# Kernel optimization log

Measured on AMD Instinct MI355X. Metric: run time of the kernel, lower is better.

Reference implementation:

```python
import jax, jax.numpy as jnp
import numpy as np

D_MODEL = 1024
NUM_HEADS = 16
NUM_KV_HEADS = 4
HEAD_DIM = D_MODEL // NUM_HEADS  # 64
THETA = 10000.0
MAX_SEQ_LEN = 4096


def _rope_tables(max_seq_len, d_k, theta):
    k_vec = jnp.arange(0, d_k, 2, dtype=jnp.float32) / d_k
    freq = 1.0 / (theta ** k_vec)                       # (d_k/2,)
    ang = jnp.arange(max_seq_len, dtype=jnp.float32)[:, None] * freq[None, :]
    return jnp.cos(ang), jnp.sin(ang)                   # each (max_seq_len, d_k/2)


def _apply_rope(x, pos, cos_table, sin_table):
    # x: (b, h, l, d), pos: (b, l)
    cos = cos_table[pos][:, None, :, :]                 # (b, 1, l, d/2)
    sin = sin_table[pos][:, None, :, :]
    even, odd = x[..., 0::2], x[..., 1::2]
    r1 = even * cos - odd * sin
    r2 = even * sin + odd * cos
    return jnp.stack([r1, r2], axis=-1).reshape(x.shape)  # interleave back


def setup_inputs() -> dict:
    key = jax.random.key(0)
    ks = jax.random.split(key, 6)
    B, L, D = 1, 4096, D_MODEL
    std = (2.0 / (D + D)) ** 0.5
    std_kv = (2.0 / (D + HEAD_DIM * NUM_KV_HEADS)) ** 0.5
    x = jax.random.normal(ks[0], (B, L, D), dtype=jnp.float32)
    Wq = jax.random.normal(ks[1], (D, D), dtype=jnp.float32) * std
    Wk = jax.random.normal(ks[2], (HEAD_DIM * NUM_KV_HEADS, D), dtype=jnp.float32) * std_kv
    Wv = jax.random.normal(ks[3], (HEAD_DIM * NUM_KV_HEADS, D), dtype=jnp.float32) * std_kv
    Wo = jax.random.normal(ks[4], (D, D), dtype=jnp.float32) * std
    token_positions = jnp.broadcast_to(jnp.arange(L, dtype=jnp.int32), (B, L))
    return {"x": x, "Wq": Wq, "Wk": Wk, "Wv": Wv, "Wo": Wo,
            "token_positions": token_positions}


def reference(x, Wq, Wk, Wv, Wo, token_positions):
    B, L, D = x.shape
    H, Hkv, Dh = NUM_HEADS, NUM_KV_HEADS, HEAD_DIM
    n_rep = H // Hkv
    cos_t, sin_t = _rope_tables(MAX_SEQ_LEN, Dh, THETA)

    q = (x @ Wq.T).reshape(B, L, H, Dh).transpose(0, 2, 1, 3)      # b h l d
    k = (x @ Wk.T).reshape(B, L, Hkv, Dh).transpose(0, 2, 1, 3)    # b g l d
    v = (x @ Wv.T).reshape(B, L, Hkv, Dh).transpose(0, 2, 1, 3)

    q = _apply_rope(q, token_positions, cos_t, sin_t)
    k = _apply_rope(k, token_positions, cos_t, sin_t)

    # GQA: group query heads by kv head
    qg = q.reshape(B, Hkv, n_rep, L, Dh)
    scores = jnp.einsum('bgrqd,bgkd->bgrqk', qg, k) / jnp.sqrt(jnp.float32(Dh))
    causal = jnp.tril(jnp.ones((L, L), dtype=bool))
    scores = jnp.where(causal, scores, -jnp.inf)
    weights = jax.nn.softmax(scores, axis=-1)
    out = jnp.einsum('bgrqk,bgkd->bgrqd', weights, v)              # b g r q d
    out = out.reshape(B, H, L, Dh).transpose(0, 2, 1, 3).reshape(B, L, D)
    return out @ Wo.T
```

## Files before the change

### kernel.cpp

```cpp
#include <hip/hip_runtime.h>
#include <hip/hip_bf16.h>
#include <math.h>

typedef __bf16 bf16;
typedef __bf16 v8bf __attribute__((ext_vector_type(8)));
typedef __bf16 v4bf __attribute__((ext_vector_type(4)));
typedef float f32x4 __attribute__((ext_vector_type(4)));

#define L_SEQ 4096
#define DMODEL 1024
#define NHEADS 16
#define DH 64
#define NEG_BIG (-1e30f)
#define LN1E4_64 0.14391156f

__global__ void convert_all(const float* __restrict__ x, const float* __restrict__ wq,
                            const float* __restrict__ wk, const float* __restrict__ wv,
                            const float* __restrict__ wo,
                            bf16* __restrict__ xb, bf16* __restrict__ wqkvb,
                            bf16* __restrict__ wob) {
    int i = (blockIdx.x * 256 + threadIdx.x) * 4;
    const float* src;
    bf16* dst;
    if (i < 4194304)      { src = x  + i;             dst = xb    + i; }
    else if (i < 5242880) { src = wq + (i - 4194304); dst = wqkvb + (i - 4194304); }
    else if (i < 5505024) { src = wk + (i - 5242880); dst = wqkvb + 1048576 + (i - 5242880); }
    else if (i < 5767168) { src = wv + (i - 5505024); dst = wqkvb + 1310720 + (i - 5505024); }
    else                  { src = wo + (i - 5767168); dst = wob   + (i - 5767168); }
    f32x4 v = *(const f32x4*)src;
    v4bf r;
#pragma unroll
    for (int j = 0; j < 4; j++) r[j] = (bf16)v[j];
    *(v4bf*)dst = r;
}

__global__ __launch_bounds__(512) void gemm_qkv(const bf16* __restrict__ A,
                                                const bf16* __restrict__ W,
                                                bf16* __restrict__ Qb,
                                                bf16* __restrict__ Kb,
                                                bf16* __restrict__ Vtg,
                                                const int* __restrict__ tp) {
    __shared__ bf16 As[128][68];
    __shared__ bf16 Bs[128][68];
    const int K = 1024;
    const int tid = threadIdx.x;
    const int w = tid >> 6, lane = tid & 63;
    const int quad = lane >> 4, l16 = lane & 15;
    const int wm = (w & 1) * 64, wn = (w >> 1) * 32;
    const int bm = blockIdx.y * 128, bn = blockIdx.x * 128;

    f32x4 acc[4][2];
#pragma unroll
    for (int mf = 0; mf < 4; mf++)
#pragma unroll
        for (int nf = 0; nf < 2; nf++) acc[mf][nf] = (f32x4){0.f, 0.f, 0.f, 0.f};

    const int sr = tid >> 2;
    const int scb = (tid & 3) * 16;

    v8bf pa0, pa1, pb0, pb1;
    {
        const bf16* ap = &A[(size_t)(bm + sr) * K + scb];
        const bf16* bp = &W[(size_t)(bn + sr) * K + scb];
        pa0 = *(const v8bf*)ap; pa1 = *(const v8bf*)(ap + 8);
        pb0 = *(const v8bf*)bp; pb1 = *(const v8bf*)(bp + 8);
        *(v8bf*)&As[sr][scb] = pa0; *(v8bf*)&As[sr][scb + 8] = pa1;
        *(v8bf*)&Bs[sr][scb] = pb0; *(v8bf*)&Bs[sr][scb + 8] = pb1;
    }

    for (int kt = 0; kt < K; kt += 64) {
        __syncthreads();
        const bool more = (kt + 64) < K;
        if (more) {
            const bf16* ap = &A[(size_t)(bm + sr) * K + kt + 64 + scb];
            const bf16* bp = &W[(size_t)(bn + sr) * K + kt + 64 + scb];
            pa0 = *(const v8bf*)ap; pa1 = *(const v8bf*)(ap + 8);
            pb0 = *(const v8bf*)bp; pb1 = *(const v8bf*)(bp + 8);
        }
#pragma unroll
        for (int kf = 0; kf < 2; kf++) {
            v8bf a[4], b[2];
#pragma unroll
            for (int mf = 0; mf < 4; mf++) a[mf] = *(v8bf*)&As[wm + mf * 16 + l16][kf * 32 + quad * 8];
#pragma unroll
            for (int nf = 0; nf < 2; nf++) b[nf] = *(v8bf*)&Bs[wn + nf * 16 + l16][kf * 32 + quad * 8];
#pragma unroll
            for (int mf = 0; mf < 4; mf++)
#pragma unroll
                for (int nf = 0; nf < 2; nf++)
                    acc[mf][nf] = __builtin_amdgcn_mfma_f32_16x16x32_bf16(a[mf], b[nf], acc[mf][nf], 0, 0, 0);
        }
        __syncthreads();
        if (more) {
            *(v8bf*)&As[sr][scb] = pa0; *(v8bf*)&As[sr][scb + 8] = pa1;
            *(v8bf*)&Bs[sr][scb] = pb0; *(v8bf*)&Bs[sr][scb + 8] = pb1;
        }
    }

    if (bn < 1024) {
#pragma unroll
        for (int mf = 0; mf < 4; mf++) {
            int pos_[4];
#pragma unroll
            for (int r = 0; r < 4; r++) pos_[r] = tp[bm + wm + mf * 16 + quad * 4 + r];
#pragma unroll
            for (int nf = 0; nf < 2; nf++) {
                const int col = bn + wn + nf * 16 + l16;
                float fr = __expf(-(float)((col & 63) & ~1) * LN1E4_64);
#pragma unroll
                for (int r = 0; r < 4; r++) {
                    float v = acc[mf][nf][r];
                    float sn, cs;
                    __sincosf((float)pos_[r] * fr, &sn, &cs);
                    float p = __shfl_xor(v, 1);
                    float res = (l16 & 1) ? (p * sn + v * cs) : (v * cs - p * sn);
                    int row = bm + wm + mf * 16 + quad * 4 + r;
                    Qb[(size_t)row * DMODEL + col] = (bf16)res;
                }
            }
        }
    } else if (bn < 1280) {
#pragma unroll
        for (int mf = 0; mf < 4; mf++) {
            int pos_[4];
#pragma unroll
            for (int r = 0; r < 4; r++) pos_[r] = tp[bm + wm + mf * 16 + quad * 4 + r];
#pragma unroll
            for (int nf = 0; nf < 2; nf++) {
                const int kcol = bn - 1024 + wn + nf * 16 + l16;
                float fr = __expf(-(float)((kcol & 63) & ~1) * LN1E4_64);
#pragma unroll
                for (int r = 0; r < 4; r++) {
                    float v = acc[mf][nf][r];
                    float sn, cs;
                    __sincosf((float)pos_[r] * fr, &sn, &cs);
                    float p = __shfl_xor(v, 1);
                    float res = (l16 & 1) ? (p * sn + v * cs) : (v * cs - p * sn);
                    int row = bm + wm + mf * 16 + quad * 4 + r;
                    Kb[(size_t)row * 256 + kcol] = (bf16)res;
                }
            }
        }
    } else {
#pragma unroll
        for (int mf = 0; mf < 4; mf++)
#pragma unroll
            for (int nf = 0; nf < 2; nf++) {
                v4bf pk;
#pragma unroll
                for (int r = 0; r < 4; r++) pk[r] = (bf16)acc[mf][nf][r];
                int vcol = bn - 1280 + wn + nf * 16 + l16;
                int row = bm + wm + mf * 16 + quad * 4;
                *(v4bf*)&Vtg[(size_t)vcol * L_SEQ + row] = pk;
            }
    }
}

__global__ __launch_bounds__(512) void gemm_out(const bf16* __restrict__ A,
                                                const bf16* __restrict__ W,
                                                float* __restrict__ C) {
    __shared__ bf16 As[128][68];
    __shared__ bf16 Bs[128][68];
    const int K = 1024, N = 1024;
    const int tid = threadIdx.x;
    const int w = tid >> 6, lane = tid & 63;
    const int quad = lane >> 4, l16 = lane & 15;
    const int wm = (w & 1) * 64, wn = (w >> 1) * 32;
    const int bm = blockIdx.y * 128, bn = blockIdx.x * 128;

    f32x4 acc[4][2];
#pragma unroll
    for (int mf = 0; mf < 4; mf++)
#pragma unroll
        for (int nf = 0; nf < 2; nf++) acc[mf][nf] = (f32x4){0.f, 0.f, 0.f, 0.f};

    const int sr = tid >> 2;
    const int scb = (tid & 3) * 16;

    v8bf pa0, pa1, pb0, pb1;
    {
        const bf16* ap = &A[(size_t)(bm + sr) * K + scb];
        const bf16* bp = &W[(size_t)(bn + sr) * K + scb];
        pa0 = *(const v8bf*)ap; pa1 = *(const v8bf*)(ap + 8);
        pb0 = *(const v8bf*)bp; pb1 = *(const v8bf*)(bp + 8);
        *(v8bf*)&As[sr][scb] = pa0; *(v8bf*)&As[sr][scb + 8] = pa1;
        *(v8bf*)&Bs[sr][scb] = pb0; *(v8bf*)&Bs[sr][scb + 8] = pb1;
    }

    for (int kt = 0; kt < K; kt += 64) {
        __syncthreads();
        const bool more = (kt + 64) < K;
        if (more) {
            const bf16* ap = &A[(size_t)(bm + sr) * K + kt + 64 + scb];
            const bf16* bp = &W[(size_t)(bn + sr) * K + kt + 64 + scb];
            pa0 = *(const v8bf*)ap; pa1 = *(const v8bf*)(ap + 8);
            pb0 = *(const v8bf*)bp; pb1 = *(const v8bf*)(bp + 8);
        }
#pragma unroll
        for (int kf = 0; kf < 2; kf++) {
            v8bf a[4], b[2];
#pragma unroll
            for (int mf = 0; mf < 4; mf++) a[mf] = *(v8bf*)&As[wm + mf * 16 + l16][kf * 32 + quad * 8];
#pragma unroll
            for (int nf = 0; nf < 2; nf++) b[nf] = *(v8bf*)&Bs[wn + nf * 16 + l16][kf * 32 + quad * 8];
#pragma unroll
            for (int mf = 0; mf < 4; mf++)
#pragma unroll
                for (int nf = 0; nf < 2; nf++)
                    acc[mf][nf] = __builtin_amdgcn_mfma_f32_16x16x32_bf16(a[mf], b[nf], acc[mf][nf], 0, 0, 0);
        }
        __syncthreads();
        if (more) {
            *(v8bf*)&As[sr][scb] = pa0; *(v8bf*)&As[sr][scb + 8] = pa1;
            *(v8bf*)&Bs[sr][scb] = pb0; *(v8bf*)&Bs[sr][scb + 8] = pb1;
        }
    }
#pragma unroll
    for (int mf = 0; mf < 4; mf++)
#pragma unroll
        for (int nf = 0; nf < 2; nf++)
#pragma unroll
            for (int r = 0; r < 4; r++) {
                int row = bm + wm + mf * 16 + quad * 4 + r;
                int col = bn + wn + nf * 16 + l16;
                C[(size_t)row * N + col] = acc[mf][nf][r];
            }
}

__global__ __launch_bounds__(256, 2) void flash5(const bf16* __restrict__ Q,
                                                 const bf16* __restrict__ Kb,
                                                 const bf16* __restrict__ Vtg,
                                                 bf16* __restrict__ O0,
                                                 bf16* __restrict__ O1,
                                                 float* __restrict__ ML) {
    __shared__ bf16 Ks[128][68];
    __shared__ bf16 Vt[64][132];
    __shared__ bf16 Ps[128][68];
    const int h = blockIdx.y, kvh = h >> 2;
    const int bx = blockIdx.x;
    const int tid = threadIdx.x;
    const int w = tid >> 6, lane = tid & 63;
    const int quad = lane >> 4, l16 = lane & 15;
    const int krow = tid >> 1, kcb = (tid & 1) * 32;
    const int vr = tid >> 2, vcb = (tid & 3) * 32;
    const float scl = 0.125f;

    for (int p = 0; p < 2; p++) {
        const int qb = p ? (31 - bx) : bx;
        const int T = qb + 1;
        const int k0 = p ? ((T + 1) >> 1) : 0;
        const int k1 = p ? T : ((T + 1) >> 1);
        bf16* Op = p ? O1 : O0;
        float* mlp = ML + (size_t)(p * NHEADS + h) * L_SEQ * 2;

        if (k0 >= k1) {
            for (int i = tid; i < 128 * 64; i += 256) {
                int rr = i >> 6, cc = i & 63;
                Op[(size_t)(qb * 128 + rr) * DMODEL + h * DH + cc] = (bf16)0.f;
            }
            if (tid < 128) {
                mlp[(qb * 128 + tid) * 2 + 0] = NEG_BIG;
                mlp[(qb * 128 + tid) * 2 + 1] = 0.f;
            }
            continue;
        }

        v8bf qf[2][2];
#pragma unroll
        for (int mf = 0; mf < 2; mf++)
#pragma unroll
            for (int kf = 0; kf < 2; kf++)
                qf[mf][kf] = *(const v8bf*)&Q[(size_t)(qb * 128 + w * 32 + mf * 16 + l16) * DMODEL
                                              + h * DH + kf * 32 + quad * 8];

        f32x4 oacc[2][4];
#pragma unroll
        for (int mf = 0; mf < 2; mf++)
#pragma unroll
            for (int d = 0; d < 4; d++) oacc[mf][d] = (f32x4){0.f, 0.f, 0.f, 0.f};
        float m_i[2][4], l_i[2][4];
#pragma unroll
        for (int mf = 0; mf < 2; mf++)
#pragma unroll
            for (int r = 0; r < 4; r++) { m_i[mf][r] = NEG_BIG; l_i[mf][r] = 0.f; }

        v8bf kreg[4], vreg[4];
        {
            const bf16* ks = &Kb[(size_t)(k0 * 128 + krow) * 256 + kvh * DH + kcb];
            const bf16* vs = &Vtg[(size_t)(kvh * DH + vr) * L_SEQ + k0 * 128 + vcb];
#pragma unroll
            for (int u = 0; u < 4; u++) { kreg[u] = *(const v8bf*)&ks[8 * u]; vreg[u] = *(const v8bf*)&vs[8 * u]; }
            __syncthreads();
#pragma unroll
            for (int u = 0; u < 4; u++) { *(v8bf*)&Ks[krow][kcb + 8 * u] = kreg[u]; *(v8bf*)&Vt[vr][vcb + 8 * u] = vreg[u]; }
        }

        for (int kb = k0; kb < k1; kb++) {
            __syncthreads();
            if (kb + 1 < k1) {
                const bf16* ks = &Kb[(size_t)((kb + 1) * 128 + krow) * 256 + kvh * DH + kcb];
                const bf16* vs = &Vtg[(size_t)(kvh * DH + vr) * L_SEQ + (kb + 1) * 128 + vcb];
#pragma unroll
                for (int u = 0; u < 4; u++) { kreg[u] = *(const v8bf*)&ks[8 * u]; vreg[u] = *(const v8bf*)&vs[8 * u]; }
            }

            f32x4 s[2][8];
#pragma unroll
            for (int n = 0; n < 8; n++) {
                v8bf b0 = *(v8bf*)&Ks[n * 16 + l16][quad * 8];
                v8bf b1 = *(v8bf*)&Ks[n * 16 + l16][32 + quad * 8];
#pragma unroll
                for (int mf = 0; mf < 2; mf++) {
                    s[mf][n] = (f32x4){0.f, 0.f, 0.f, 0.f};
                    s[mf][n] = __builtin_amdgcn_mfma_f32_16x16x32_bf16(qf[mf][0], b0, s[mf][n], 0, 0, 0);
                    s[mf][n] = __builtin_amdgcn_mfma_f32_16x16x32_bf16(qf[mf][1], b1, s[mf][n], 0, 0, 0);
                }
            }

            if (kb == qb) {
#pragma unroll
                for (int mf = 0; mf < 2; mf++) {
                    int rbase = qb * 128 + w * 32 + mf * 16 + quad * 4;
#pragma unroll
                    for (int n = 0; n < 8; n++) {
                        int colg = kb * 128 + n * 16 + l16;
#pragma unroll
                        for (int r = 0; r < 4; r++)
                            s[mf][n][r] = (colg <= rbase + r) ? s[mf][n][r] * scl : NEG_BIG;
                    }
                }
            } else {
#pragma unroll
                for (int mf = 0; mf < 2; mf++)
#pragma unroll
                    for (int n = 0; n < 8; n++)
#pragma unroll
                        for (int r = 0; r < 4; r++) s[mf][n][r] *= scl;
            }

            float mx[2][4];
#pragma unroll
            for (int mf = 0; mf < 2; mf++)
#pragma unroll
                for (int r = 0; r < 4; r++) {
                    float m0 = s[mf][0][r];
#pragma unroll
                    for (int n = 1; n < 8; n++) m0 = fmaxf(m0, s[mf][n][r]);
                    mx[mf][r] = m0;
                }
#pragma unroll
            for (int off = 1; off < 16; off <<= 1)
#pragma unroll
                for (int mf = 0; mf < 2; mf++)
#pragma unroll
                    for (int r = 0; r < 4; r++)
                        mx[mf][r] = fmaxf(mx[mf][r], __shfl_xor(mx[mf][r], off));

            float alpha[2][4], mnew[2][4], rs[2][4];
#pragma unroll
            for (int mf = 0; mf < 2; mf++)
#pragma unroll
                for (int r = 0; r < 4; r++) {
                    mnew[mf][r]  = fmaxf(m_i[mf][r], mx[mf][r]);
                    alpha[mf][r] = __expf(m_i[mf][r] - mnew[mf][r]);
                    rs[mf][r] = 0.f;
                }
#pragma unroll
            for (int mf = 0; mf < 2; mf++)
#pragma unroll
                for (int n = 0; n < 8; n++)
#pragma unroll
                    for (int r = 0; r < 4; r++) {
                        float pv = __expf(s[mf][n][r] - mnew[mf][r]);
                        s[mf][n][r] = pv;
                        rs[mf][r] += pv;
                    }
#pragma unroll
            for (int off = 1; off < 16; off <<= 1)
#pragma unroll
                for (int mf = 0; mf < 2; mf++)
#pragma unroll
                    for (int r = 0; r < 4; r++) rs[mf][r] += __shfl_xor(rs[mf][r], off);
#pragma unroll
            for (int mf = 0; mf < 2; mf++)
#pragma unroll
                for (int r = 0; r < 4; r++) {
                    l_i[mf][r] = l_i[mf][r] * alpha[mf][r] + rs[mf][r];
                    m_i[mf][r] = mnew[mf][r];
                }
#pragma unroll
            for (int mf = 0; mf < 2; mf++)
#pragma unroll
                for (int d = 0; d < 4; d++)
#pragma unroll
                    for (int r = 0; r < 4; r++) oacc[mf][d][r] *= alpha[mf][r];

#pragma unroll
            for (int half = 0; half < 2; half++) {
#pragma unroll
                for (int mf = 0; mf < 2; mf++)
#pragma unroll
                    for (int n = 0; n < 4; n++)
#pragma unroll
                        for (int r = 0; r < 4; r++)
                            Ps[w * 32 + mf * 16 + quad * 4 + r][n * 16 + l16] =
                                (bf16)s[mf][half * 4 + n][r];
#pragma unroll
                for (int kf = 0; kf < 2; kf++) {
#pragma unroll
                    for (int mf = 0; mf < 2; mf++) {
                        v8bf pa = *(v8bf*)&Ps[w * 32 + mf * 16 + l16][kf * 32 + quad * 8];
#pragma unroll
                        for (int d = 0; d < 4; d++) {
                            v8bf vb = *(v8bf*)&Vt[d * 16 + l16][half * 64 + kf * 32 + quad * 8];
                            oacc[mf][d] = __builtin_amdgcn_mfma_f32_16x16x32_bf16(pa, vb, oacc[mf][d], 0, 0, 0);
                        }
                    }
                }
            }

            __syncthreads();
            if (kb + 1 < k1) {
#pragma unroll
                for (int u = 0; u < 4; u++) { *(v8bf*)&Ks[krow][kcb + 8 * u] = kreg[u]; *(v8bf*)&Vt[vr][vcb + 8 * u] = vreg[u]; }
            }
        }

#pragma unroll
        for (int mf = 0; mf < 2; mf++)
#pragma unroll
            for (int d = 0; d < 4; d++)
#pragma unroll
                for (int r = 0; r < 4; r++) {
                    int row = qb * 128 + w * 32 + mf * 16 + quad * 4 + r;
                    Op[(size_t)row * DMODEL + h * DH + d * 16 + l16] = (bf16)oacc[mf][d][r];
                }
        if (l16 == 0) {
#pragma unroll
            for (int mf = 0; mf < 2; mf++)
#pragma unroll
                for (int r = 0; r < 4; r++) {
                    int row = qb * 128 + w * 32 + mf * 16 + quad * 4 + r;
                    mlp[row * 2 + 0] = m_i[mf][r];
                    mlp[row * 2 + 1] = l_i[mf][r];
                }
        }
    }
}

__global__ void combine(const bf16* __restrict__ O0, const bf16* __restrict__ O1,
                        const float* __restrict__ ML, bf16* __restrict__ Attn) {
    int gid = blockIdx.x * 256 + threadIdx.x;
    int row = gid >> 8;
    int cg = (gid & 255) * 4;
    int h = cg >> 6;
    const float* ml0 = ML + ((size_t)h * L_SEQ + row) * 2;
    const float* ml1 = ML + ((size_t)(NHEADS + h) * L_SEQ + row) * 2;
    float m0 = ml0[0], l0 = ml0[1], m1 = ml1[0], l1 = ml1[1];
    float m = fmaxf(m0, m1);
    float a0 = __expf(m0 - m), a1 = __expf(m1 - m);
    float inv = 1.f / (a0 * l0 + a1 * l1);
    v4bf o0 = *(const v4bf*)&O0[(size_t)row * DMODEL + cg];
    v4bf o1 = *(const v4bf*)&O1[(size_t)row * DMODEL + cg];
    v4bf res;
#pragma unroll
    for (int j = 0; j < 4; j++)
        res[j] = (bf16)((a0 * (float)o0[j] + a1 * (float)o1[j]) * inv);
    *(v4bf*)&Attn[(size_t)row * DMODEL + cg] = res;
}

extern "C" void kernel_launch(void* const* d_in, const int* in_sizes, int n_in,
                              void* d_out, int out_size, void* d_ws, size_t ws_size,
                              hipStream_t stream) {
    const float* x  = (const float*)d_in[0];
    const float* Wq = (const float*)d_in[1];
    const float* Wk = (const float*)d_in[2];
    const float* Wv = (const float*)d_in[3];
    const float* Wo = (const float*)d_in[4];
    const int*   tp = (const int*)d_in[5];
    float* out = (float*)d_out;

    bf16*  xb    = (bf16*)d_ws;
    bf16*  wqkvb = xb    + 4194304;
    bf16*  wob   = wqkvb + 1572864;
    bf16*  Qb    = wob   + 1048576;
    bf16*  Kb    = Qb    + 4194304;
    bf16*  Vtg   = Kb    + 1048576;
    float* MLf   = (float*)(Vtg + 1048576);
    bf16*  Attn  = xb;
    bf16*  O0    = (bf16*)d_out;
    bf16*  O1    = O0 + 4194304;

    convert_all<<<6656, 256, 0, stream>>>(x, Wq, Wk, Wv, Wo, xb, wqkvb, wob);
    gemm_qkv<<<dim3(12, 32), 512, 0, stream>>>(xb, wqkvb, Qb, Kb, Vtg, tp);
    flash5<<<dim3(32, NHEADS), 256, 0, stream>>>(Qb, Kb, Vtg, O0, O1, MLf);
    combine<<<4096, 256, 0, stream>>>(O0, O1, MLf, Attn);
    gemm_out<<<dim3(8, 32), 512, 0, stream>>>(Attn, wob, out);
}
```

Before: 226.6 us.

## Use 8 waves of 16 query rows per flash block with exp2 softmax and setprio

Flash attention now runs 512 threads per block, with each of 8 waves owning 16 query rows instead of 4 waves owning 32. This halves per-thread register state and the cooperative K/V load work, which should allow more waves in flight to hide latency. Softmax switches to exp2 with the log2(e) factor folded into the score scale, and the combine kernel uses exp2 to match. s_setprio is raised around the MFMA sections. The trade-off is more waves contending for the same LDS tiles and barriers.

```diff
diff --git a/kernel.cpp b/kernel.cpp
--- a/kernel.cpp
+++ b/kernel.cpp
@@ -13,6 +13,7 @@
 #define DH 64
 #define NEG_BIG (-1e30f)
 #define LN1E4_64 0.14391156f
+#define SCL2 0.18033688f
 
 __global__ void convert_all(const float* __restrict__ x, const float* __restrict__ wq,
                             const float* __restrict__ wk, const float* __restrict__ wv,
@@ -227,7 +228,7 @@
             }
 }
 
-__global__ __launch_bounds__(256, 2) void flash5(const bf16* __restrict__ Q,
+__global__ __launch_bounds__(512, 4) void flash6(const bf16* __restrict__ Q,
                                                  const bf16* __restrict__ Kb,
                                                  const bf16* __restrict__ Vtg,
                                                  bf16* __restrict__ O0,
@@ -241,9 +242,8 @@
     const int tid = threadIdx.x;
     const int w = tid >> 6, lane = tid & 63;
     const int quad = lane >> 4, l16 = lane & 15;
-    const int krow = tid >> 1, kcb = (tid & 1) * 32;
-    const int vr = tid >> 2, vcb = (tid & 3) * 32;
-    const float scl = 0.125f;
+    const int krow = tid >> 2, kcb = (tid & 3) * 16;
+    const int vr = tid >> 3, vcb = (tid & 7) * 16;
 
     for (int p = 0; p < 2; p++) {
         const int qb = p ? (31 - bx) : bx;
@@ -254,7 +254,7 @@
         float* mlp = ML + (size_t)(p * NHEADS + h) * L_SEQ * 2;
 
         if (k0 >= k1) {
-            for (int i = tid; i < 128 * 64; i += 256) {
+            for (int i = tid; i < 128 * 64; i += 512) {
                 int rr = i >> 6, cc = i & 63;
                 Op[(size_t)(qb * 128 + rr) * DMODEL + h * DH + cc] = (bf16)0.f;
             }
@@ -265,34 +265,28 @@
             continue;
         }
 
-        v8bf qf[2][2];
-#pragma unroll
-        for (int mf = 0; mf < 2; mf++)
-#pragma unroll
-            for (int kf = 0; kf < 2; kf++)
-                qf[mf][kf] = *(const v8bf*)&Q[(size_t)(qb * 128 + w * 32 + mf * 16 + l16) * DMODEL
-                                              + h * DH + kf * 32 + quad * 8];
-
-        f32x4 oacc[2][4];
-#pragma unroll
-        for (int mf = 0; mf < 2; mf++)
-#pragma unroll
-            for (int d = 0; d < 4; d++) oacc[mf][d] = (f32x4){0.f, 0.f, 0.f, 0.f};
-        float m_i[2][4], l_i[2][4];
-#pragma unroll
-        for (int mf = 0; mf < 2; mf++)
-#pragma unroll
-            for (int r = 0; r < 4; r++) { m_i[mf][r] = NEG_BIG; l_i[mf][r] = 0.f; }
-
-        v8bf kreg[4], vreg[4];
+        v8bf qf[2];
+#pragma unroll
+        for (int kf = 0; kf < 2; kf++)
+            qf[kf] = *(const v8bf*)&Q[(size_t)(qb * 128 + w * 16 + l16) * DMODEL
+                                      + h * DH + kf * 32 + quad * 8];
+
+        f32x4 oacc[4];
+#pragma unroll
+        for (int d = 0; d < 4; d++) oacc[d] = (f32x4){0.f, 0.f, 0.f, 0.f};
+        float m_i[4], l_i[4];
+#pragma unroll
+        for (int r = 0; r < 4; r++) { m_i[r] = NEG_BIG; l_i[r] = 0.f; }
+
+        v8bf kreg[2], vreg[2];
         {
             const bf16* ks = &Kb[(size_t)(k0 * 128 + krow) * 256 + kvh * DH + kcb];
             const bf16* vs = &Vtg[(size_t)(kvh * DH + vr) * L_SEQ + k0 * 128 + vcb];
-#pragma unroll
-            for (int u = 0; u < 4; u++) { kreg[u] = *(const v8bf*)&ks[8 * u]; vreg[u] = *(const v8bf*)&vs[8 * u]; }
+            kreg[0] = *(const v8bf*)ks; kreg[1] = *(const v8bf*)(ks + 8);
+            vreg[0] = *(const v8bf*)vs; vreg[1] = *(const v8bf*)(vs + 8);
             __syncthreads();
-#pragma unroll
-            for (int u = 0; u < 4; u++) { *(v8bf*)&Ks[krow][kcb + 8 * u] = kreg[u]; *(v8bf*)&Vt[vr][vcb + 8 * u] = vreg[u]; }
+            *(v8bf*)&Ks[krow][kcb] = kreg[0]; *(v8bf*)&Ks[krow][kcb + 8] = kreg[1];
+            *(v8bf*)&Vt[vr][vcb] = vreg[0];   *(v8bf*)&Vt[vr][vcb + 8] = vreg[1];
         }
 
         for (int kb = k0; kb < k1; kb++) {
@@ -300,150 +294,122 @@
             if (kb + 1 < k1) {
                 const bf16* ks = &Kb[(size_t)((kb + 1) * 128 + krow) * 256 + kvh * DH + kcb];
                 const bf16* vs = &Vtg[(size_t)(kvh * DH + vr) * L_SEQ + (kb + 1) * 128 + vcb];
-#pragma unroll
-                for (int u = 0; u < 4; u++) { kreg[u] = *(const v8bf*)&ks[8 * u]; vreg[u] = *(const v8bf*)&vs[8 * u]; }
-            }
-
-            f32x4 s[2][8];
+                kreg[0] = *(const v8bf*)ks; kreg[1] = *(const v8bf*)(ks + 8);
+                vreg[0] = *(const v8bf*)vs; vreg[1] = *(const v8bf*)(vs + 8);
+            }
+
+            f32x4 s[8];
+            __builtin_amdgcn_s_setprio(1);
 #pragma unroll
             for (int n = 0; n < 8; n++) {
                 v8bf b0 = *(v8bf*)&Ks[n * 16 + l16][quad * 8];
                 v8bf b1 = *(v8bf*)&Ks[n * 16 + l16][32 + quad * 8];
-#pragma unroll
-                for (int mf = 0; mf < 2; mf++) {
-                    s[mf][n] = (f32x4){0.f, 0.f, 0.f, 0.f};
-                    s[mf][n] = __builtin_amdgcn_mfma_f32_16x16x32_bf16(qf[mf][0], b0, s[mf][n], 0, 0, 0);
-                    s[mf][n] = __builtin_amdgcn_mfma_f32_16x16x32_bf16(qf[mf][1], b1, s[mf][n], 0, 0, 0);
+                s[n] = (f32x4){0.f, 0.f, 0.f, 0.f};
+                s[n] = __builtin_amdgcn_mfma_f32_16x16x32_bf16(qf[0], b0, s[n], 0, 0, 0);
+                s[n] = __builtin_amdgcn_mfma_f32_16x16x32_bf16(qf[1], b1, s[n], 0, 0, 0);
+            }
+            __builtin_amdgcn_s_setprio(0);
+
+            if (kb == qb) {
+                int rbase = qb * 128 + w * 16 + quad * 4;
+#pragma unroll
+                for (int n = 0; n < 8; n++) {
+                    int colg = kb * 128 + n * 16 + l16;
+#pragma unroll
+                    for (int r = 0; r < 4; r++)
+                        s[n][r] = (colg <= rbase + r) ? s[n][r] * SCL2 : NEG_BIG;
                 }
-            }
-
-            if (kb == qb) {
-#pragma unroll
-                for (int mf = 0; mf < 2; mf++) {
-                    int rbase = qb * 128 + w * 32 + mf * 16 + quad * 4;
-#pragma unroll
-                    for (int n = 0; n < 8; n++) {
-                        int colg = kb * 128 + n * 16 + l16;
-#pragma unroll
-                        for (int r = 0; r < 4; r++)
-                            s[mf][n][r] = (colg <= rbase + r) ? s[mf][n][r] * scl : NEG_BIG;
+            } else {
+#pragma unroll
+                for (int n = 0; n < 8; n++)
+#pragma unroll
+                    for (int r = 0; r < 4; r++) s[n][r] *= SCL2;
+            }
+
+            float mx[4];
+#pragma unroll
+            for (int r = 0; r < 4; r++) {
+                float m0 = s[0][r];
+#pragma unroll
+                for (int n = 1; n < 8; n++) m0 = fmaxf(m0, s[n][r]);
+                mx[r] = m0;
+            }
+#pragma unroll
+            for (int off = 1; off < 16; off <<= 1)
+#pragma unroll
+                for (int r = 0; r < 4; r++)
+                    mx[r] = fmaxf(mx[r], __shfl_xor(mx[r], off));
+
+            float alpha[4], mnew[4], rs[4];
+#pragma unroll
+            for (int r = 0; r < 4; r++) {
+                mnew[r]  = fmaxf(m_i[r], mx[r]);
+                alpha[r] = exp2f(m_i[r] - mnew[r]);
+                rs[r] = 0.f;
+            }
+#pragma unroll
+            for (int n = 0; n < 8; n++)
+#pragma unroll
+                for (int r = 0; r < 4; r++) {
+                    float pv = exp2f(s[n][r] - mnew[r]);
+                    s[n][r] = pv;
+                    rs[r] += pv;
+                }
+#pragma unroll
+            for (int off = 1; off < 16; off <<= 1)
+#pragma unroll
+                for (int r = 0; r < 4; r++) rs[r] += __shfl_xor(rs[r], off);
+#pragma unroll
+            for (int r = 0; r < 4; r++) {
+                l_i[r] = l_i[r] * alpha[r] + rs[r];
+                m_i[r] = mnew[r];
+            }
+#pragma unroll
+            for (int d = 0; d < 4; d++)
+#pragma unroll
+                for (int r = 0; r < 4; r++) oacc[d][r] *= alpha[r];
+
+#pragma unroll
+            for (int half = 0; half < 2; half++) {
+#pragma unroll
+                for (int n = 0; n < 4; n++)
+#pragma unroll
+                    for (int r = 0; r < 4; r++)
+                        Ps[w * 16 + quad * 4 + r][n * 16 + l16] = (bf16)s[half * 4 + n][r];
+                __builtin_amdgcn_s_setprio(1);
+#pragma unroll
+                for (int kf = 0; kf < 2; kf++) {
+                    v8bf pa = *(v8bf*)&Ps[w * 16 + l16][kf * 32 + quad * 8];
+#pragma unroll
+                    for (int d = 0; d < 4; d++) {
+                        v8bf vb = *(v8bf*)&Vt[d * 16 + l16][half * 64 + kf * 32 + quad * 8];
+                        oacc[d] = __builtin_amdgcn_mfma_f32_16x16x32_bf16(pa, vb, oacc[d], 0, 0, 0);
                     }
                 }
-            } else {
-#pragma unroll
-                for (int mf = 0; mf < 2; mf++)
-#pragma unroll
-                    for (int n = 0; n < 8; n++)
-#pragma unroll
-                        for (int r = 0; r < 4; r++) s[mf][n][r] *= scl;
-            }
-
-            float mx[2][4];
-#pragma unroll
-            for (int mf = 0; mf < 2; mf++)
-#pragma unroll
-                for (int r = 0; r < 4; r++) {
-                    float m0 = s[mf][0][r];
-#pragma unroll
-                    for (int n = 1; n < 8; n++) m0 = fmaxf(m0, s[mf][n][r]);
-                    mx[mf][r] = m0;
-                }
-#pragma unroll
-            for (int off = 1; off < 16; off <<= 1)
-#pragma unroll
-                for (int mf = 0; mf < 2; mf++)
-#pragma unroll
-                    for (int r = 0; r < 4; r++)
-                        mx[mf][r] = fmaxf(mx[mf][r], __shfl_xor(mx[mf][r], off));
-
-            float alpha[2][4], mnew[2][4], rs[2][4];
-#pragma unroll
-            for (int mf = 0; mf < 2; mf++)
-#pragma unroll
-                for (int r = 0; r < 4; r++) {
-                    mnew[mf][r]  = fmaxf(m_i[mf][r], mx[mf][r]);
-                    alpha[mf][r] = __expf(m_i[mf][r] - mnew[mf][r]);
-                    rs[mf][r] = 0.f;
-                }
-#pragma unroll
-            for (int mf = 0; mf < 2; mf++)
-#pragma unroll
-                for (int n = 0; n < 8; n++)
-#pragma unroll
-                    for (int r = 0; r < 4; r++) {
-                        float pv = __expf(s[mf][n][r] - mnew[mf][r]);
-                        s[mf][n][r] = pv;
-                        rs[mf][r] += pv;
-                    }
-#pragma unroll
-            for (int off = 1; off < 16; off <<= 1)
-#pragma unroll
-                for (int mf = 0; mf < 2; mf++)
-#pragma unroll
-                    for (int r = 0; r < 4; r++) rs[mf][r] += __shfl_xor(rs[mf][r], off);
-#pragma unroll
-            for (int mf = 0; mf < 2; mf++)
-#pragma unroll
-                for (int r = 0; r < 4; r++) {
-                    l_i[mf][r] = l_i[mf][r] * alpha[mf][r] + rs[mf][r];
-                    m_i[mf][r] = mnew[mf][r];
-                }
-#pragma unroll
-            for (int mf = 0; mf < 2; mf++)
-#pragma unroll
-                for (int d = 0; d < 4; d++)
-#pragma unroll
-                    for (int r = 0; r < 4; r++) oacc[mf][d][r] *= alpha[mf][r];
-
-#pragma unroll
-            for (int half = 0; half < 2; half++) {
-#pragma unroll
-                for (int mf = 0; mf < 2; mf++)
-#pragma unroll
-                    for (int n = 0; n < 4; n++)
-#pragma unroll
-                        for (int r = 0; r < 4; r++)
-                            Ps[w * 32 + mf * 16 + quad * 4 + r][n * 16 + l16] =
-                                (bf16)s[mf][half * 4 + n][r];
-#pragma unroll
-                for (int kf = 0; kf < 2; kf++) {
-#pragma unroll
-                    for (int mf = 0; mf < 2; mf++) {
-                        v8bf pa = *(v8bf*)&Ps[w * 32 + mf * 16 + l16][kf * 32 + quad * 8];
-#pragma unroll
-                        for (int d = 0; d < 4; d++) {
-                            v8bf vb = *(v8bf*)&Vt[d * 16 + l16][half * 64 + kf * 32 + quad * 8];
-                            oacc[mf][d] = __builtin_amdgcn_mfma_f32_16x16x32_bf16(pa, vb, oacc[mf][d], 0, 0, 0);
-                        }
-                    }
-                }
+                __builtin_amdgcn_s_setprio(0);
             }
 
             __syncthreads();
             if (kb + 1 < k1) {
-#pragma unroll
-                for (int u = 0; u < 4; u++) { *(v8bf*)&Ks[krow][kcb + 8 * u] = kreg[u]; *(v8bf*)&Vt[vr][vcb + 8 * u] = vreg[u]; }
-            }
-        }
-
-#pragma unroll
-        for (int mf = 0; mf < 2; mf++)
-#pragma unroll
-            for (int d = 0; d < 4; d++)
-#pragma unroll
-                for (int r = 0; r < 4; r++) {
-                    int row = qb * 128 + w * 32 + mf * 16 + quad * 4 + r;
-                    Op[(size_t)row * DMODEL + h * DH + d * 16 + l16] = (bf16)oacc[mf][d][r];
-                }
+                *(v8bf*)&Ks[krow][kcb] = kreg[0]; *(v8bf*)&Ks[krow][kcb + 8] = kreg[1];
+                *(v8bf*)&Vt[vr][vcb] = vreg[0];   *(v8bf*)&Vt[vr][vcb + 8] = vreg[1];
+            }
+        }
+
+#pragma unroll
+        for (int d = 0; d < 4; d++)
+#pragma unroll
+            for (int r = 0; r < 4; r++) {
+                int row = qb * 128 + w * 16 + quad * 4 + r;
+                Op[(size_t)row * DMODEL + h * DH + d * 16 + l16] = (bf16)oacc[d][r];
+            }
         if (l16 == 0) {
 #pragma unroll
-            for (int mf = 0; mf < 2; mf++)
-#pragma unroll
-                for (int r = 0; r < 4; r++) {
-                    int row = qb * 128 + w * 32 + mf * 16 + quad * 4 + r;
-                    mlp[row * 2 + 0] = m_i[mf][r];
-                    mlp[row * 2 + 1] = l_i[mf][r];
-                }
+            for (int r = 0; r < 4; r++) {
+                int row = qb * 128 + w * 16 + quad * 4 + r;
+                mlp[row * 2 + 0] = m_i[r];
+                mlp[row * 2 + 1] = l_i[r];
+            }
         }
     }
 }
@@ -458,7 +424,7 @@
     const float* ml1 = ML + ((size_t)(NHEADS + h) * L_SEQ + row) * 2;
     float m0 = ml0[0], l0 = ml0[1], m1 = ml1[0], l1 = ml1[1];
     float m = fmaxf(m0, m1);
-    float a0 = __expf(m0 - m), a1 = __expf(m1 - m);
+    float a0 = exp2f(m0 - m), a1 = exp2f(m1 - m);
     float inv = 1.f / (a0 * l0 + a1 * l1);
     v4bf o0 = *(const v4bf*)&O0[(size_t)row * DMODEL + cg];
     v4bf o1 = *(const v4bf*)&O1[(size_t)row * DMODEL + cg];
@@ -493,7 +459,7 @@
 
     convert_all<<<6656, 256, 0, stream>>>(x, Wq, Wk, Wv, Wo, xb, wqkvb, wob);
     gemm_qkv<<<dim3(12, 32), 512, 0, stream>>>(xb, wqkvb, Qb, Kb, Vtg, tp);
-    flash5<<<dim3(32, NHEADS), 256, 0, stream>>>(Qb, Kb, Vtg, O0, O1, MLf);
+    flash6<<<dim3(32, NHEADS), 512, 0, stream>>>(Qb, Kb, Vtg, O0, O1, MLf);
     combine<<<4096, 256, 0, stream>>>(O0, O1, MLf, Attn);
     gemm_out<<<dim3(8, 32), 512, 0, stream>>>(Attn, wob, out);
 }
```

After: 247.3 us. +9.1%, slower.
